# Performance work log

Measured on AMD Instinct MI355X. Metric: run time of the kernel, lower is better.

Reference implementation:

```python
import jax, jax.numpy as jnp
import numpy as np

B, CIN, COUT, K, KN, HID, HW = 16, 256, 256, 3, 4, 16, 64
PAD = K // 2
EPS = 1e-5


def setup_inputs() -> dict:
    key = jax.random.key(0)
    ks = jax.random.split(key, 6)
    x = jax.random.normal(ks[0], (B, CIN, HW, HW), dtype=jnp.float32)
    # attention MLP: 1x1 conv -> BN -> ReLU -> 1x1 conv (on 1x1 pooled maps == dense)
    w1 = jax.random.normal(ks[1], (HID, CIN), dtype=jnp.float32) * (1.0 / np.sqrt(CIN))
    bn_gamma = jnp.ones((HID,), dtype=jnp.float32)
    bn_beta = jnp.zeros((HID,), dtype=jnp.float32)
    bn_mean = jnp.zeros((HID,), dtype=jnp.float32)
    bn_var = jnp.ones((HID,), dtype=jnp.float32)
    w2 = jax.random.normal(ks[2], (KN, HID), dtype=jnp.float32) * (1.0 / np.sqrt(HID))
    # kaiming-normal fan_out: std = sqrt(2 / (Cout * k * k))
    weight = jax.random.normal(ks[3], (KN, COUT, CIN, K, K), dtype=jnp.float32) * np.sqrt(2.0 / (COUT * K * K))
    return {"x": x, "w1": w1, "bn_gamma": bn_gamma, "bn_beta": bn_beta,
            "bn_mean": bn_mean, "bn_var": bn_var, "w2": w2, "weight": weight}


def reference(x, w1, bn_gamma, bn_beta, bn_mean, bn_var, w2, weight):
    b = x.shape[0]
    # global average pool -> [B, Cin]
    pooled = jnp.mean(x, axis=(2, 3))
    h = pooled @ w1.T                                   # [B, HID]
    h = (h - bn_mean) * jax.lax.rsqrt(bn_var + EPS) * bn_gamma + bn_beta
    h = jax.nn.relu(h)
    att = jax.nn.softmax(h @ w2.T, axis=1)              # [B, KN]
    # aggregate per-sample kernels: [B, Cout, Cin, K, K]
    agg_w = jnp.einsum('bk,koijl->boijl', att, weight)
    # batched dynamic conv via batch-as-groups grouped conv
    x_g = x.reshape(1, b * CIN, x.shape[2], x.shape[3])
    w_g = agg_w.reshape(b * COUT, CIN, K, K)
    out = jax.lax.conv_general_dilated(
        x_g, w_g, window_strides=(1, 1), padding=[(PAD, PAD), (PAD, PAD)],
        dimension_numbers=('NCHW', 'OIHW', 'NCHW'), feature_group_count=b)
    return out.reshape(b, COUT, out.shape[2], out.shape[3])
```

## Files before the change

kernel.cpp:

```cpp
#include <hip/hip_runtime.h>

typedef __attribute__((ext_vector_type(8))) short bf16x8;
typedef __attribute__((ext_vector_type(4))) float f32x4;

#define AS3 __attribute__((address_space(3)))
#define AS1 __attribute__((address_space(1)))

__device__ __forceinline__ unsigned short f2bf(float f) {
  unsigned u = __float_as_uint(f);
  u += 0x7fffu + ((u >> 16) & 1u);
  return (unsigned short)(u >> 16);
}

__global__ void transpose_kernel(const float* __restrict__ x,
                                 unsigned short* __restrict__ xTp,
                                 float* __restrict__ pooled) {
  __shared__ unsigned short tb[64][258];
  const int blk = blockIdx.x;
  const int b = blk >> 6, y = blk & 63;
  const int t = threadIdx.x;
  const int xcol = t & 63;
  const int cbase = t >> 6;
  const float* src = x + (size_t)b * 256 * 4096 + (size_t)y * 64;
  for (int it = 0; it < 64; ++it) {
    const int c = it * 4 + cbase;
    tb[xcol][c] = f2bf(src[(size_t)c * 4096 + xcol]);
  }
  __syncthreads();
  unsigned short* dst = xTp + (size_t)b * (4356 * 256) + ((size_t)(y + 1) * 66 + 1) * 256;
  float psum = 0.f;
  for (int xx = 0; xx < 64; ++xx) {
    const unsigned short v = tb[xx][t];
    psum += __uint_as_float((unsigned)v << 16);
    dst[(size_t)xx * 256 + t] = v;
  }
  atomicAdd(&pooled[b * 256 + t], psum * (1.0f / 4096.0f));
}

__global__ void border_kernel(unsigned short* __restrict__ xTp) {
  const int br = blockIdx.x;
  const int b = blockIdx.y;
  int y, xx;
  if (br < 66) { y = 0; xx = br; }
  else if (br < 132) { y = 65; xx = br - 66; }
  else { const int k = br - 132; y = 1 + (k >> 1); xx = (k & 1) * 65; }
  xTp[((size_t)b * 4356 + y * 66 + xx) * 256 + threadIdx.x] = 0;
}

__global__ void attn_kernel(const float* __restrict__ pooled,
                            const float* __restrict__ w1,
                            const float* __restrict__ bng,
                            const float* __restrict__ bnb,
                            const float* __restrict__ bnm,
                            const float* __restrict__ bnv,
                            const float* __restrict__ w2,
                            float* __restrict__ att) {
  __shared__ float hbuf[256];
  const int t = threadIdx.x;
  const int b = t >> 4, i = t & 15;
  float s = 0.f;
  for (int c = 0; c < 256; ++c) s += pooled[b * 256 + c] * w1[i * 256 + c];
  float h = (s - bnm[i]) * rsqrtf(bnv[i] + 1e-5f) * bng[i] + bnb[i];
  hbuf[t] = fmaxf(h, 0.f);
  __syncthreads();
  if (t < 64) {
    const int bb = t >> 2, k = t & 3;
    float l = 0.f;
    for (int j = 0; j < 16; ++j) l += hbuf[bb * 16 + j] * w2[k * 16 + j];
    float m = l;
    m = fmaxf(m, __shfl_xor(m, 1, 64));
    m = fmaxf(m, __shfl_xor(m, 2, 64));
    float e = expf(l - m);
    float sum = e;
    sum += __shfl_xor(sum, 1, 64);
    sum += __shfl_xor(sum, 2, 64);
    att[bb * 4 + k] = e / sum;
  }
}

__global__ void agg_kernel(const float* __restrict__ att,
                           const float* __restrict__ wgt,
                           unsigned short* __restrict__ agg) {
  const int bo = blockIdx.x;
  const int b = bo >> 8, o = bo & 255;
  const int c = threadIdx.x;
  float acc[9];
#pragma unroll
  for (int t = 0; t < 9; ++t) acc[t] = 0.f;
#pragma unroll
  for (int k = 0; k < 4; ++k) {
    const float ak = att[b * 4 + k];
    const float* wp = wgt + ((size_t)((k << 8) + o) * 256 + c) * 9;
#pragma unroll
    for (int t = 0; t < 9; ++t) acc[t] += ak * wp[t];
  }
#pragma unroll
  for (int t = 0; t < 9; ++t)
    agg[(((size_t)(b * 9 + t) * 256) + o) * 256 + c] = f2bf(acc[t]);
}

__global__ __launch_bounds__(512, 2) void conv_kernel(
    const unsigned short* __restrict__ xTp,
    const unsigned short* __restrict__ agg,
    float* __restrict__ out) {
  __shared__ unsigned short ldsA[4 * 256 * 32];
  __shared__ unsigned short ldsB[4 * 256 * 32];

  const int bid = blockIdx.x;
  const int b = bid & 15;
  const int mt = bid >> 4;
  const int p0 = mt << 8;
  const int y0 = mt << 2;

  const int tid = threadIdx.x;
  const int lane = tid & 63;
  const int wave = tid >> 6;
  const int wm = wave >> 2;
  const int wn = wave & 3;

  const int srow = tid >> 2;
  const int scol = (tid & 3) << 3;
  int baseA[2], baseB[2];
#pragma unroll
  for (int issue = 0; issue < 2; ++issue) {
    const int r = srow + (issue << 7);
    baseA[issue] = ((y0 + (r >> 6)) * 66 + (r & 63)) * 256 + scol;
    baseB[issue] = (b * 2304 + r) * 256 + scol;
  }

  const unsigned short* xb = xTp + (size_t)b * (4356 * 256);
  AS3 char* ldsA3 = (AS3 char*)ldsA;
  AS3 char* ldsB3 = (AS3 char*)ldsB;

  auto stage = [&](int ks_) {
    const int kss = ks_ > 71 ? 71 : ks_;
    const int slotb = (ks_ & 3) << 14;
    const int tap = kss >> 3;
    const int dy = tap / 3;
    const int dx = tap - dy * 3;
    const int c0 = (kss & 7) << 5;
    const int offA = (dy * 66 + dx) * 256 + c0;
    const int offB = (tap << 16) + c0;
#pragma unroll
    for (int issue = 0; issue < 2; ++issue) {
      __builtin_amdgcn_global_load_lds(
          (const AS1 void*)(xb + baseA[issue] + offA),
          (AS3 void*)(ldsA3 + slotb + (issue << 13) + (wave << 10)), 16, 0, 0);
      __builtin_amdgcn_global_load_lds(
          (const AS1 void*)(agg + baseB[issue] + offB),
          (AS3 void*)(ldsB3 + slotb + (issue << 13) + (wave << 10)), 16, 0, 0);
    }
  };

  const int l15 = lane & 15;
  const int lhi = lane >> 4;
  int aoff[8], boff[4];
#pragma unroll
  for (int m = 0; m < 8; ++m) aoff[m] = (wm * 128 + m * 16 + l15) * 64 + lhi * 16;
#pragma unroll
  for (int n = 0; n < 4; ++n) boff[n] = (wn * 64 + n * 16 + l15) * 64 + lhi * 16;

  f32x4 acc[8][4];
#pragma unroll
  for (int m = 0; m < 8; ++m)
#pragma unroll
    for (int n = 0; n < 4; ++n) acc[m][n] = (f32x4){0.f, 0.f, 0.f, 0.f};

  stage(0);
  stage(1);
  stage(2);

#pragma unroll 1
  for (int ks = 0; ks < 72; ++ks) {
    asm volatile("s_waitcnt vmcnt(8)" ::: "memory");
    __builtin_amdgcn_s_barrier();
    __builtin_amdgcn_sched_barrier(0);
    const int slotb = (ks & 3) << 14;
    bf16x8 af[8], bfr[4];
#pragma unroll
    for (int m = 0; m < 8; ++m)
      af[m] = *reinterpret_cast<const bf16x8*>((const char*)ldsA + slotb + aoff[m]);
#pragma unroll
    for (int n = 0; n < 4; ++n)
      bfr[n] = *reinterpret_cast<const bf16x8*>((const char*)ldsB + slotb + boff[n]);
    stage(ks + 3);
    __builtin_amdgcn_s_setprio(1);
#pragma unroll
    for (int m = 0; m < 8; ++m)
#pragma unroll
      for (int n = 0; n < 4; ++n)
        acc[m][n] = __builtin_amdgcn_mfma_f32_16x16x32_bf16(af[m], bfr[n],
                                                            acc[m][n], 0, 0, 0);
    __builtin_amdgcn_s_setprio(0);
  }

#pragma unroll
  for (int m = 0; m < 8; ++m) {
    const int p = p0 + wm * 128 + m * 16 + (lhi << 2);
#pragma unroll
    for (int n = 0; n < 4; ++n) {
      const int co = wn * 64 + n * 16 + l15;
      float* dst = out + ((size_t)(b * 256 + co) << 12) + p;
      *reinterpret_cast<f32x4*>(dst) = acc[m][n];
    }
  }
}

extern "C" void kernel_launch(void* const* d_in, const int* in_sizes, int n_in,
                              void* d_out, int out_size, void* d_ws, size_t ws_size,
                              hipStream_t stream) {
  const float* x = (const float*)d_in[0];
  const float* w1 = (const float*)d_in[1];
  const float* bng = (const float*)d_in[2];
  const float* bnb = (const float*)d_in[3];
  const float* bnm = (const float*)d_in[4];
  const float* bnv = (const float*)d_in[5];
  const float* w2 = (const float*)d_in[6];
  const float* wgt = (const float*)d_in[7];
  float* out = (float*)d_out;

  char* ws = (char*)d_ws;
  const size_t xtp_bytes = (size_t)16 * 4356 * 256 * 2;
  const size_t agg_bytes = (size_t)16 * 9 * 256 * 256 * 2;
  unsigned short* xTp = (unsigned short*)ws;
  unsigned short* agg = (unsigned short*)(ws + xtp_bytes);
  float* pooled = (float*)(ws + xtp_bytes + agg_bytes);
  float* att = (float*)(ws + xtp_bytes + agg_bytes + 16384);

  hipMemsetAsync(pooled, 0, 16 * 256 * sizeof(float), stream);
  border_kernel<<<dim3(260, 16), 256, 0, stream>>>(xTp);
  transpose_kernel<<<1024, 256, 0, stream>>>(x, xTp, pooled);
  attn_kernel<<<1, 256, 0, stream>>>(pooled, w1, bng, bnb, bnm, bnv, w2, att);
  agg_kernel<<<4096, 256, 0, stream>>>(att, wgt, agg);
  conv_kernel<<<256, 512, 0, stream>>>(xTp, agg, out);
}
```

Before: 126.9 us.

## Restructure conv to reuse a haloed input tile across taps; split Cout across blocks

The conv kernel now loads a haloed input slab (4 image rows plus halo) into LDS once per 32-channel chunk and reuses it across all 9 taps. Only the weight tiles are streamed, through a 4-slot ring, with XOR-swizzled LDS addressing. Output channels are split in half across blocks, giving 512 blocks with smaller 4x4 per-wave accumulators and higher launch-bounds occupancy. Separately, agg_kernel reads the four weight banks once per output channel and loops over the batch, and the transpose writeback is vectorized to 4 channels per thread. The tap loop has more barriers and a full vmcnt(0) wait per chunk, which may stall.

```diff
diff --git a/kernel.cpp b/kernel.cpp
--- a/kernel.cpp
+++ b/kernel.cpp
@@ -10,6 +10,9 @@
   unsigned u = __float_as_uint(f);
   u += 0x7fffu + ((u >> 16) & 1u);
   return (unsigned short)(u >> 16);
+}
+__device__ __forceinline__ float bf2f(unsigned short v) {
+  return __uint_as_float((unsigned)v << 16);
 }
 
 __global__ void transpose_kernel(const float* __restrict__ x,
@@ -28,13 +31,20 @@
   }
   __syncthreads();
   unsigned short* dst = xTp + (size_t)b * (4356 * 256) + ((size_t)(y + 1) * 66 + 1) * 256;
-  float psum = 0.f;
-  for (int xx = 0; xx < 64; ++xx) {
-    const unsigned short v = tb[xx][t];
-    psum += __uint_as_float((unsigned)v << 16);
-    dst[(size_t)xx * 256 + t] = v;
-  }
-  atomicAdd(&pooled[b * 256 + t], psum * (1.0f / 4096.0f));
+  const int wv = t >> 6, ln = t & 63;
+  float p0 = 0.f, p1 = 0.f, p2 = 0.f, p3 = 0.f;
+  for (int i = 0; i < 16; ++i) {
+    const int xx = wv * 16 + i;
+    ushort2 v0 = *(const ushort2*)&tb[xx][ln * 4];
+    ushort2 v1 = *(const ushort2*)&tb[xx][ln * 4 + 2];
+    p0 += bf2f(v0.x); p1 += bf2f(v0.y); p2 += bf2f(v1.x); p3 += bf2f(v1.y);
+    ushort4 v = {v0.x, v0.y, v1.x, v1.y};
+    *(ushort4*)&dst[(size_t)xx * 256 + ln * 4] = v;
+  }
+  atomicAdd(&pooled[b * 256 + ln * 4 + 0], p0 * (1.0f / 4096.0f));
+  atomicAdd(&pooled[b * 256 + ln * 4 + 1], p1 * (1.0f / 4096.0f));
+  atomicAdd(&pooled[b * 256 + ln * 4 + 2], p2 * (1.0f / 4096.0f));
+  atomicAdd(&pooled[b * 256 + ln * 4 + 3], p3 * (1.0f / 4096.0f));
 }
 
 __global__ void border_kernel(unsigned short* __restrict__ xTp) {
@@ -81,125 +91,145 @@
 __global__ void agg_kernel(const float* __restrict__ att,
                            const float* __restrict__ wgt,
                            unsigned short* __restrict__ agg) {
-  const int bo = blockIdx.x;
-  const int b = bo >> 8, o = bo & 255;
+  const int o = blockIdx.x;
   const int c = threadIdx.x;
-  float acc[9];
-#pragma unroll
-  for (int t = 0; t < 9; ++t) acc[t] = 0.f;
+  float w[4][9];
 #pragma unroll
   for (int k = 0; k < 4; ++k) {
-    const float ak = att[b * 4 + k];
     const float* wp = wgt + ((size_t)((k << 8) + o) * 256 + c) * 9;
 #pragma unroll
-    for (int t = 0; t < 9; ++t) acc[t] += ak * wp[t];
-  }
-#pragma unroll
-  for (int t = 0; t < 9; ++t)
-    agg[(((size_t)(b * 9 + t) * 256) + o) * 256 + c] = f2bf(acc[t]);
-}
-
-__global__ __launch_bounds__(512, 2) void conv_kernel(
+    for (int t = 0; t < 9; ++t) w[k][t] = wp[t];
+  }
+  __shared__ float attS[64];
+  if (c < 64) attS[c] = att[c];
+  __syncthreads();
+#pragma unroll 1
+  for (int b = 0; b < 16; ++b) {
+    const float a0 = attS[b * 4 + 0], a1 = attS[b * 4 + 1];
+    const float a2 = attS[b * 4 + 2], a3 = attS[b * 4 + 3];
+#pragma unroll
+    for (int t = 0; t < 9; ++t) {
+      const float v = a0 * w[0][t] + a1 * w[1][t] + a2 * w[2][t] + a3 * w[3][t];
+      agg[(((size_t)(b * 9 + t) * 256) + o) * 256 + c] = f2bf(v);
+    }
+  }
+}
+
+__global__ __launch_bounds__(512, 4) void conv_kernel(
     const unsigned short* __restrict__ xTp,
     const unsigned short* __restrict__ agg,
     float* __restrict__ out) {
-  __shared__ unsigned short ldsA[4 * 256 * 32];
-  __shared__ unsigned short ldsB[4 * 256 * 32];
+  __shared__ unsigned short lds[512 * 32 + 4 * 128 * 32];
+  AS3 char* ldsA3 = (AS3 char*)lds;
+  AS3 char* ldsB3 = (AS3 char*)(lds + 512 * 32);
 
   const int bid = blockIdx.x;
   const int b = bid & 15;
-  const int mt = bid >> 4;
+  const int rest = bid >> 4;
+  const int mt = rest >> 1;
+  const int nh = rest & 1;
   const int p0 = mt << 8;
-  const int y0 = mt << 2;
+  const int rowA0 = mt * 264;
 
   const int tid = threadIdx.x;
   const int lane = tid & 63;
   const int wave = tid >> 6;
-  const int wm = wave >> 2;
-  const int wn = wave & 3;
+  const int wm = wave >> 1;
+  const int wn = wave & 1;
 
   const int srow = tid >> 2;
-  const int scol = (tid & 3) << 3;
-  int baseA[2], baseB[2];
-#pragma unroll
-  for (int issue = 0; issue < 2; ++issue) {
-    const int r = srow + (issue << 7);
-    baseA[issue] = ((y0 + (r >> 6)) * 66 + (r & 63)) * 256 + scol;
-    baseB[issue] = (b * 2304 + r) * 256 + scol;
-  }
-
-  const unsigned short* xb = xTp + (size_t)b * (4356 * 256);
-  AS3 char* ldsA3 = (AS3 char*)ldsA;
-  AS3 char* ldsB3 = (AS3 char*)ldsB;
-
-  auto stage = [&](int ks_) {
-    const int kss = ks_ > 71 ? 71 : ks_;
-    const int slotb = (ks_ & 3) << 14;
-    const int tap = kss >> 3;
-    const int dy = tap / 3;
-    const int dx = tap - dy * 3;
-    const int c0 = (kss & 7) << 5;
-    const int offA = (dy * 66 + dx) * 256 + c0;
-    const int offB = (tap << 16) + c0;
-#pragma unroll
-    for (int issue = 0; issue < 2; ++issue) {
+  const int scol = ((tid & 3) ^ ((tid >> 3) & 3)) << 3;
+  const int sdst = srow * 64 + (tid & 3) * 16;
+
+  const unsigned short* xbs =
+      xTp + (size_t)b * (4356 * 256) + (size_t)rowA0 * 256 + scol;
+  const unsigned short* aggs =
+      agg + ((size_t)(b * 9) * 256 + nh * 128 + srow) * 256 + scol;
+
+  auto stageA = [&](int c0) {
+#pragma unroll
+    for (int i = 0; i < 4; ++i) {
+      const int h = srow + (i << 7);
+      const int hs = h > 395 ? 395 : h;
       __builtin_amdgcn_global_load_lds(
-          (const AS1 void*)(xb + baseA[issue] + offA),
-          (AS3 void*)(ldsA3 + slotb + (issue << 13) + (wave << 10)), 16, 0, 0);
-      __builtin_amdgcn_global_load_lds(
-          (const AS1 void*)(agg + baseB[issue] + offB),
-          (AS3 void*)(ldsB3 + slotb + (issue << 13) + (wave << 10)), 16, 0, 0);
-    }
+          (const AS1 void*)(xbs + (size_t)hs * 256 + c0 * 32),
+          (AS3 void*)(ldsA3 + sdst + (i << 13)), 16, 0, 0);
+    }
+  };
+  auto stageB = [&](int c02, int tap2, int slot) {
+    __builtin_amdgcn_global_load_lds(
+        (const AS1 void*)(aggs + tap2 * 65536 + c02 * 32),
+        (AS3 void*)(ldsB3 + slot * 8192 + sdst), 16, 0, 0);
   };
 
   const int l15 = lane & 15;
   const int lhi = lane >> 4;
-  int aoff[8], boff[4];
-#pragma unroll
-  for (int m = 0; m < 8; ++m) aoff[m] = (wm * 128 + m * 16 + l15) * 64 + lhi * 16;
-#pragma unroll
-  for (int n = 0; n < 4; ++n) boff[n] = (wn * 64 + n * 16 + l15) * 64 + lhi * 16;
-
-  f32x4 acc[8][4];
-#pragma unroll
-  for (int m = 0; m < 8; ++m)
+  const int hb = wm * 66 + l15;
+  const int rslotB = (lhi ^ ((l15 >> 1) & 3)) << 4;
+  int boffs[4];
+#pragma unroll
+  for (int n = 0; n < 4; ++n)
+    boffs[n] = 32768 * 2  + (wn * 64 + n * 16 + l15) * 64 + rslotB;
+#pragma unroll
+  for (int n = 0; n < 4; ++n)
+    boffs[n] = 32768 + (wn * 64 + n * 16 + l15) * 64 + rslotB;
+
+  f32x4 acc[4][4];
+#pragma unroll
+  for (int m = 0; m < 4; ++m)
 #pragma unroll
     for (int n = 0; n < 4; ++n) acc[m][n] = (f32x4){0.f, 0.f, 0.f, 0.f};
 
-  stage(0);
-  stage(1);
-  stage(2);
+  stageB(0, 0, 0);
+  stageB(0, 1, 1);
 
 #pragma unroll 1
-  for (int ks = 0; ks < 72; ++ks) {
-    asm volatile("s_waitcnt vmcnt(8)" ::: "memory");
+  for (int c0 = 0; c0 < 8; ++c0) {
     __builtin_amdgcn_s_barrier();
-    __builtin_amdgcn_sched_barrier(0);
-    const int slotb = (ks & 3) << 14;
-    bf16x8 af[8], bfr[4];
-#pragma unroll
-    for (int m = 0; m < 8; ++m)
-      af[m] = *reinterpret_cast<const bf16x8*>((const char*)ldsA + slotb + aoff[m]);
-#pragma unroll
-    for (int n = 0; n < 4; ++n)
-      bfr[n] = *reinterpret_cast<const bf16x8*>((const char*)ldsB + slotb + boff[n]);
-    stage(ks + 3);
-    __builtin_amdgcn_s_setprio(1);
-#pragma unroll
-    for (int m = 0; m < 8; ++m)
+    stageA(c0);
+    asm volatile("s_waitcnt vmcnt(0)" ::: "memory");
+    __builtin_amdgcn_s_barrier();
+#pragma unroll
+    for (int tap = 0; tap < 9; ++tap) {
+      if (tap != 0) {
+        asm volatile("s_waitcnt vmcnt(1)" ::: "memory");
+        __builtin_amdgcn_s_barrier();
+      }
+      __builtin_amdgcn_sched_barrier(0);
+      const int dy = tap / 3, dx = tap % 3;
+      const int slotR = (c0 + tap) & 3;
+      bf16x8 af[4], bfr[4];
+#pragma unroll
+      for (int m = 0; m < 4; ++m) {
+        const int h = hb + dy * 66 + dx + m * 16;
+        const int ab = h * 64 + ((lhi ^ ((h >> 1) & 3)) << 4);
+        af[m] = *(const bf16x8*)((const char*)lds + ab);
+      }
 #pragma unroll
       for (int n = 0; n < 4; ++n)
-        acc[m][n] = __builtin_amdgcn_mfma_f32_16x16x32_bf16(af[m], bfr[n],
-                                                            acc[m][n], 0, 0, 0);
-    __builtin_amdgcn_s_setprio(0);
-  }
-
-#pragma unroll
-  for (int m = 0; m < 8; ++m) {
-    const int p = p0 + wm * 128 + m * 16 + (lhi << 2);
+        bfr[n] = *(const bf16x8*)((const char*)lds + slotR * 8192 + boffs[n]);
+      int c02, tap2;
+      if (tap <= 6) { c02 = c0; tap2 = tap + 2; }
+      else { c02 = c0 + 1; tap2 = tap - 7; }
+      if (c02 > 7) { c02 = 7; tap2 = 8; }
+      stageB(c02, tap2, (c0 + tap + 2) & 3);
+      __builtin_amdgcn_s_setprio(1);
+#pragma unroll
+      for (int m = 0; m < 4; ++m)
+#pragma unroll
+        for (int n = 0; n < 4; ++n)
+          acc[m][n] = __builtin_amdgcn_mfma_f32_16x16x32_bf16(af[m], bfr[n],
+                                                              acc[m][n], 0, 0, 0);
+      __builtin_amdgcn_s_setprio(0);
+    }
+  }
+
+#pragma unroll
+  for (int m = 0; m < 4; ++m) {
+    const int p = p0 + wm * 64 + m * 16 + (lhi << 2);
 #pragma unroll
     for (int n = 0; n < 4; ++n) {
-      const int co = wn * 64 + n * 16 + l15;
+      const int co = nh * 128 + wn * 64 + n * 16 + l15;
       float* dst = out + ((size_t)(b * 256 + co) << 12) + p;
       *reinterpret_cast<f32x4*>(dst) = acc[m][n];
     }
@@ -231,6 +261,6 @@
   border_kernel<<<dim3(260, 16), 256, 0, stream>>>(xTp);
   transpose_kernel<<<1024, 256, 0, stream>>>(x, xTp, pooled);
   attn_kernel<<<1, 256, 0, stream>>>(pooled, w1, bng, bnb, bnm, bnv, w2, att);
-  agg_kernel<<<4096, 256, 0, stream>>>(att, wgt, agg);
-  conv_kernel<<<256, 512, 0, stream>>>(xTp, agg, out);
-}
+  agg_kernel<<<256, 256, 0, stream>>>(att, wgt, agg);
+  conv_kernel<<<512, 512, 0, stream>>>(xTp, agg, out);
+}
```

Result: slower. 165.6 us (+30.5%).
